# Optimization experiments

Hardware: AMD Instinct MI355X
Metric: run time of the kernel (lower is better)

The kernel has to match this reference:

```python
import jax, jax.numpy as jnp
import numpy as np

B, NCAP, LEN, CDF = 8, 4, 1024, 768
NUM, IDF = 1024, 512


def setup_inputs() -> dict:
    key = jax.random.key(0)
    k1, k2, k3 = jax.random.split(key, 3)
    obj = jax.random.normal(k1, (B, NUM, IDF), dtype=jnp.float32)
    text = jax.random.normal(k2, (B, NCAP, LEN, CDF), dtype=jnp.float32)
    # Linear(cdf=768 -> idf=512); kaiming-uniform-ish scale
    W = jax.random.normal(k3, (CDF, IDF), dtype=jnp.float32) / np.sqrt(CDF)
    b = jnp.zeros((IDF,), dtype=jnp.float32)
    return {"obj": obj, "text": text, "W": W, "b": b}


def reference(obj, text, W, b):
    # obj: [B, num, idf]; text: [B, 4, len, cdf]
    batch = text.shape[0]
    idf = obj.shape[2]
    # conv_context: Linear(cdf -> idf), then flatten captions: [B, L=4*len, idf]
    t = (jnp.einsum('bcle,ed->bcld', text, W) + b).reshape(batch, -1, idf)
    # unscaled, unmasked cross-attention scores: [B, num, L]
    attn = jnp.einsum('bnd,bld->bnl', obj, t)
    # softmax over the flattened text dim (nn.Softmax on 2D applies to last dim)
    attn = jax.nn.softmax(attn, axis=-1)
    # dropout(p=0.5) is identity in eval mode (deterministic reference)
    # weightedText = bmm(t^T, attn^T) then transpose -> [B, num, idf]
    out = jnp.einsum('bnl,bld->bnd', attn, t)
    return out
```

## Files before the change

kernel.cpp:

```cpp
#include <hip/hip_runtime.h>
#include <math.h>


typedef unsigned short u16;
typedef u16   u16x4  __attribute__((ext_vector_type(4)));
typedef u16   u16x8  __attribute__((ext_vector_type(8)));
typedef __bf16 bf16x8 __attribute__((ext_vector_type(8)));
typedef float f32x4  __attribute__((ext_vector_type(4)));

__device__ inline void split4(const float4 v, u16x4* h4, u16x4* l4) {
  const float xs[4] = {v.x, v.y, v.z, v.w};
  #pragma unroll
  for (int c = 0; c < 4; c++) {
    __bf16 hb = (__bf16)xs[c];
    __bf16 lb = (__bf16)(xs[c] - (float)hb);
    (*h4)[c] = __builtin_bit_cast(u16, hb);
    (*l4)[c] = __builtin_bit_cast(u16, lb);
  }
}

template<bool ADD_BIAS>
__global__ __launch_bounds__(256, 2) void gemm_nt_bf16x3(
    const float* __restrict__ A, const float* __restrict__ B,
    float* __restrict__ C, const float* __restrict__ bias,
    int M, int N, int K, long sA, long sB, long sC)
{
  __shared__ __align__(16) u16 Ah[2][128][40];
  __shared__ __align__(16) u16 Al[2][128][40];
  __shared__ __align__(16) u16 Bh[2][128][40];
  __shared__ __align__(16) u16 Bl[2][128][40];

  const float* Ab = A + (long)blockIdx.z * sA;
  const float* Bb = B + (long)blockIdx.z * sB;
  float*       Cb = C + (long)blockIdx.z * sC;

  const int m0 = blockIdx.y * 128;
  const int n0 = blockIdx.x * 128;
  const int t    = threadIdx.x;
  const int lane = t & 63;
  const int w    = t >> 6;
  const int wm   = w >> 1;
  const int wn   = w & 1;
  const int lr   = lane & 15;
  const int lg   = lane >> 4;

  f32x4 acc[4][4];
  #pragma unroll
  for (int i = 0; i < 4; i++)
    #pragma unroll
    for (int j = 0; j < 4; j++) acc[i][j] = (f32x4){0.f, 0.f, 0.f, 0.f};

  float4 av[4], bv[4];

  #define LOADK(K0)                                                                 \
    _Pragma("unroll")                                                               \
    for (int i = 0; i < 4; i++) {                                                   \
      const int f   = t + 256 * i;                                                  \
      const int row = f >> 3;                                                       \
      const int kq  = (f & 7) * 4;                                                  \
      av[i] = *reinterpret_cast<const float4*>(Ab + (long)(m0 + row) * K + (K0) + kq); \
      bv[i] = *reinterpret_cast<const float4*>(Bb + (long)(n0 + row) * K + (K0) + kq); \
    }

  #define CONVWRITE(BUF)                                                            \
    _Pragma("unroll")                                                               \
    for (int i = 0; i < 4; i++) {                                                   \
      const int f   = t + 256 * i;                                                  \
      const int row = f >> 3;                                                       \
      const int kq  = (f & 7) * 4;                                                  \
      u16x4 h4, l4;                                                                 \
      split4(av[i], &h4, &l4);                                                      \
      *reinterpret_cast<u16x4*>(&Ah[BUF][row][kq]) = h4;                            \
      *reinterpret_cast<u16x4*>(&Al[BUF][row][kq]) = l4;                            \
      split4(bv[i], &h4, &l4);                                                      \
      *reinterpret_cast<u16x4*>(&Bh[BUF][row][kq]) = h4;                            \
      *reinterpret_cast<u16x4*>(&Bl[BUF][row][kq]) = l4;                            \
    }

  LOADK(0)
  CONVWRITE(0)
  __syncthreads();

  const int nk = K >> 5;
  for (int kt = 0; kt < nk; ++kt) {
    const int cur = kt & 1;
    if (kt + 1 < nk) { LOADK((kt + 1) << 5) }

    bf16x8 afh[4], afl[4];
    #pragma unroll
    for (int i = 0; i < 4; i++) {
      const int ar = wm * 64 + i * 16 + lr;
      afh[i] = __builtin_bit_cast(bf16x8, *reinterpret_cast<const u16x8*>(&Ah[cur][ar][lg * 8]));
      afl[i] = __builtin_bit_cast(bf16x8, *reinterpret_cast<const u16x8*>(&Al[cur][ar][lg * 8]));
    }
    #pragma unroll
    for (int j = 0; j < 4; j++) {
      const int br = wn * 64 + j * 16 + lr;
      bf16x8 bh = __builtin_bit_cast(bf16x8, *reinterpret_cast<const u16x8*>(&Bh[cur][br][lg * 8]));
      bf16x8 bl = __builtin_bit_cast(bf16x8, *reinterpret_cast<const u16x8*>(&Bl[cur][br][lg * 8]));
      #pragma unroll
      for (int i = 0; i < 4; i++) {
        acc[i][j] = __builtin_amdgcn_mfma_f32_16x16x32_bf16(afl[i], bh, acc[i][j], 0, 0, 0);
        acc[i][j] = __builtin_amdgcn_mfma_f32_16x16x32_bf16(afh[i], bl, acc[i][j], 0, 0, 0);
        acc[i][j] = __builtin_amdgcn_mfma_f32_16x16x32_bf16(afh[i], bh, acc[i][j], 0, 0, 0);
      }
    }

    if (kt + 1 < nk) { CONVWRITE(cur ^ 1) }
    __syncthreads();
  }
  #undef LOADK
  #undef CONVWRITE

  #pragma unroll
  for (int j = 0; j < 4; j++) {
    const int col = n0 + wn * 64 + j * 16 + lr;
    const float bj = ADD_BIAS ? bias[col] : 0.f;
    #pragma unroll
    for (int i = 0; i < 4; i++) {
      const int row = m0 + wm * 64 + i * 16 + lg * 4;
      #pragma unroll
      for (int r = 0; r < 4; r++)
        Cb[(long)(row + r) * N + col] = acc[i][j][r] + bj;
    }
  }
}

__global__ __launch_bounds__(256) void transpose_f32(
    const float* __restrict__ in, float* __restrict__ out,
    int R, int C, long sIn, long sOut)
{
  __shared__ float tile[32][33];
  in  += (long)blockIdx.z * sIn;
  out += (long)blockIdx.z * sOut;
  const int c  = blockIdx.x * 32 + threadIdx.x;
  const int r0 = blockIdx.y * 32 + threadIdx.y;
  #pragma unroll
  for (int j = 0; j < 32; j += 8)
    tile[threadIdx.y + j][threadIdx.x] = in[(long)(r0 + j) * C + c];
  __syncthreads();
  const int c2 = blockIdx.y * 32 + threadIdx.x;
  const int r2 = blockIdx.x * 32 + threadIdx.y;
  #pragma unroll
  for (int j = 0; j < 32; j += 8)
    out[(long)(r2 + j) * R + c2] = tile[threadIdx.x][threadIdx.y + j];
}

__device__ inline float wave_max(float x) {
  #pragma unroll
  for (int o = 1; o < 64; o <<= 1) x = fmaxf(x, __shfl_xor(x, o, 64));
  return x;
}
__device__ inline float wave_sum(float x) {
  #pragma unroll
  for (int o = 1; o < 64; o <<= 1) x += __shfl_xor(x, o, 64);
  return x;
}

__global__ __launch_bounds__(256) void softmax4096_kernel(float* __restrict__ attn)
{
  __shared__ float red[4];
  float* p = attn + (long)blockIdx.x * 4096;
  const int t = threadIdx.x;

  float4 v[4];
  float mx = -3.4e38f;
  #pragma unroll
  for (int i = 0; i < 4; i++) {
    v[i] = *reinterpret_cast<const float4*>(p + i * 1024 + t * 4);
    mx = fmaxf(mx, fmaxf(fmaxf(v[i].x, v[i].y), fmaxf(v[i].z, v[i].w)));
  }
  mx = wave_max(mx);
  if ((t & 63) == 0) red[t >> 6] = mx;
  __syncthreads();
  mx = fmaxf(fmaxf(red[0], red[1]), fmaxf(red[2], red[3]));
  __syncthreads();

  float s = 0.f;
  #pragma unroll
  for (int i = 0; i < 4; i++) {
    v[i].x = __expf(v[i].x - mx); s += v[i].x;
    v[i].y = __expf(v[i].y - mx); s += v[i].y;
    v[i].z = __expf(v[i].z - mx); s += v[i].z;
    v[i].w = __expf(v[i].w - mx); s += v[i].w;
  }
  s = wave_sum(s);
  if ((t & 63) == 0) red[t >> 6] = s;
  __syncthreads();
  const float r = 1.f / (red[0] + red[1] + red[2] + red[3]);

  #pragma unroll
  for (int i = 0; i < 4; i++) {
    v[i].x *= r; v[i].y *= r; v[i].z *= r; v[i].w *= r;
    *reinterpret_cast<float4*>(p + i * 1024 + t * 4) = v[i];
  }
}

extern "C" void kernel_launch(void* const* d_in, const int* in_sizes, int n_in,
                              void* d_out, int out_size, void* d_ws, size_t ws_size,
                              hipStream_t stream)
{
  const float* obj  = (const float*)d_in[0];
  const float* text = (const float*)d_in[1];
  const float* W    = (const float*)d_in[2];
  const float* bias = (const float*)d_in[3];
  float*       out  = (float*)d_out;

  float* t    = (float*)d_ws;
  float* attn = t    + 32768L * 512;
  float* tT   = attn + 8L * 1024 * 4096;
  float* WT   = tT   + 8L * 512 * 4096;

  transpose_f32<<<dim3(512 / 32, 768 / 32, 1), dim3(32, 8), 0, stream>>>(
      W, WT, 768, 512, 0L, 0L);
  gemm_nt_bf16x3<true><<<dim3(512 / 128, 32768 / 128, 1), 256, 0, stream>>>(
      text, WT, t, bias, 32768, 512, 768, 0L, 0L, 0L);
  transpose_f32<<<dim3(512 / 32, 4096 / 32, 8), dim3(32, 8), 0, stream>>>(
      t, tT, 4096, 512, 4096L * 512, 512L * 4096);
  gemm_nt_bf16x3<false><<<dim3(4096 / 128, 1024 / 128, 8), 256, 0, stream>>>(
      obj, t, attn, nullptr, 1024, 4096, 512,
      1024L * 512, 4096L * 512, 1024L * 4096);
  softmax4096_kernel<<<8192, 256, 0, stream>>>(attn);
  gemm_nt_bf16x3<false><<<dim3(512 / 128, 1024 / 128, 8), 256, 0, stream>>>(
      attn, tT, out, nullptr, 1024, 512, 4096,
      1024L * 4096, 512L * 4096, 1024L * 512);
}
```

Measured before the change: 557.8 us.

## Pre-split operands to bf16 hi/lo in global memory and stage via direct-to-LDS loads

Operands are now converted once into separate bf16 high and low arrays in global memory by standalone split kernels, by the softmax, and by the first GEMM's epilogue. The GEMM then streams these arrays straight into swizzled LDS with global_load_lds, with each wave staging one of the four planes. This removes the per-tile float-to-bf16 split work and the register round-trip from the GEMM main loop, and the standalone transpose of t is dropped because the projection epilogue also writes the transposed t. The cost is extra kernel launches, extra global traffic to write and re-read the split copies, and a single workspace buffer reused for several tensors.

```diff
diff --git a/kernel.cpp b/kernel.cpp
--- a/kernel.cpp
+++ b/kernel.cpp
@@ -3,14 +3,14 @@
 
 
 typedef unsigned short u16;
-typedef u16   u16x4  __attribute__((ext_vector_type(4)));
-typedef u16   u16x8  __attribute__((ext_vector_type(8)));
+typedef u16 u16x4 __attribute__((ext_vector_type(4)));
+typedef u16 u16x8 __attribute__((ext_vector_type(8)));
 typedef __bf16 bf16x8 __attribute__((ext_vector_type(8)));
-typedef float f32x4  __attribute__((ext_vector_type(4)));
+typedef float f32x4 __attribute__((ext_vector_type(4)));
 
 __device__ inline void split4(const float4 v, u16x4* h4, u16x4* l4) {
   const float xs[4] = {v.x, v.y, v.z, v.w};
-  #pragma unroll
+#pragma unroll
   for (int c = 0; c < 4; c++) {
     __bf16 hb = (__bf16)xs[c];
     __bf16 lb = (__bf16)(xs[c] - (float)hb);
@@ -19,20 +19,22 @@
   }
 }
 
-template<bool ADD_BIAS>
-__global__ __launch_bounds__(256, 2) void gemm_nt_bf16x3(
-    const float* __restrict__ A, const float* __restrict__ B,
+__device__ inline void gload_lds16(const u16* g, u16* l) {
+  __builtin_amdgcn_global_load_lds(
+      (const __attribute__((address_space(1))) unsigned int*)g,
+      (__attribute__((address_space(3))) unsigned int*)l, 16, 0, 0);
+}
+
+template<int MODE>
+__global__ __launch_bounds__(256, 2) void gemm_x3(
+    const u16* __restrict__ Ah, const u16* __restrict__ Al,
+    const u16* __restrict__ Bh, const u16* __restrict__ Bl,
     float* __restrict__ C, const float* __restrict__ bias,
+    u16* __restrict__ th, u16* __restrict__ tl,
+    u16* __restrict__ tTh, u16* __restrict__ tTl,
     int M, int N, int K, long sA, long sB, long sC)
 {
-  __shared__ __align__(16) u16 Ah[2][128][40];
-  __shared__ __align__(16) u16 Al[2][128][40];
-  __shared__ __align__(16) u16 Bh[2][128][40];
-  __shared__ __align__(16) u16 Bl[2][128][40];
-
-  const float* Ab = A + (long)blockIdx.z * sA;
-  const float* Bb = B + (long)blockIdx.z * sB;
-  float*       Cb = C + (long)blockIdx.z * sC;
+  __shared__ __align__(16) u16 sh[4][2][4096];
 
   const int m0 = blockIdx.y * 128;
   const int n0 = blockIdx.x * 128;
@@ -44,128 +46,182 @@
   const int lr   = lane & 15;
   const int lg   = lane >> 4;
 
+  const u16* Abh = Ah + (long)blockIdx.z * sA;
+  const u16* Abl = Al + (long)blockIdx.z * sA;
+  const u16* Bbh = Bh + (long)blockIdx.z * sB;
+  const u16* Bbl = Bl + (long)blockIdx.z * sB;
+  float*     Cb  = C  + (long)blockIdx.z * sC;
+
+  const u16* wsrc; long wrow;
+  if      (w == 0) { wsrc = Abh; wrow = (long)m0 * K; }
+  else if (w == 1) { wsrc = Abl; wrow = (long)m0 * K; }
+  else if (w == 2) { wsrc = Bbh; wrow = (long)n0 * K; }
+  else             { wsrc = Bbl; wrow = (long)n0 * K; }
+
+  int offA[4], offB[4];
+#pragma unroll
+  for (int i = 0; i < 4; i++) {
+    const int ar = wm * 64 + i * 16 + lr;
+    offA[i] = ar * 32 + (((lg + (ar >> 1)) & 3) << 3);
+    const int br = wn * 64 + i * 16 + lr;
+    offB[i] = br * 32 + (((lg + (br >> 1)) & 3) << 3);
+  }
+
   f32x4 acc[4][4];
-  #pragma unroll
+#pragma unroll
   for (int i = 0; i < 4; i++)
-    #pragma unroll
+#pragma unroll
     for (int j = 0; j < 4; j++) acc[i][j] = (f32x4){0.f, 0.f, 0.f, 0.f};
 
-  float4 av[4], bv[4];
-
-  #define LOADK(K0)                                                                 \
-    _Pragma("unroll")                                                               \
-    for (int i = 0; i < 4; i++) {                                                   \
-      const int f   = t + 256 * i;                                                  \
-      const int row = f >> 3;                                                       \
-      const int kq  = (f & 7) * 4;                                                  \
-      av[i] = *reinterpret_cast<const float4*>(Ab + (long)(m0 + row) * K + (K0) + kq); \
-      bv[i] = *reinterpret_cast<const float4*>(Bb + (long)(n0 + row) * K + (K0) + kq); \
-    }
-
-  #define CONVWRITE(BUF)                                                            \
-    _Pragma("unroll")                                                               \
-    for (int i = 0; i < 4; i++) {                                                   \
-      const int f   = t + 256 * i;                                                  \
-      const int row = f >> 3;                                                       \
-      const int kq  = (f & 7) * 4;                                                  \
-      u16x4 h4, l4;                                                                 \
-      split4(av[i], &h4, &l4);                                                      \
-      *reinterpret_cast<u16x4*>(&Ah[BUF][row][kq]) = h4;                            \
-      *reinterpret_cast<u16x4*>(&Al[BUF][row][kq]) = l4;                            \
-      split4(bv[i], &h4, &l4);                                                      \
-      *reinterpret_cast<u16x4*>(&Bh[BUF][row][kq]) = h4;                            \
-      *reinterpret_cast<u16x4*>(&Bl[BUF][row][kq]) = l4;                            \
-    }
-
-  LOADK(0)
-  CONVWRITE(0)
+  #define STAGE(NB, K0)                                                        \
+    {                                                                          \
+      u16* lb = &sh[w][NB][0];                                                 \
+      _Pragma("unroll")                                                        \
+      for (int ii = 0; ii < 8; ii++) {                                         \
+        const int G  = ii * 64 + lane;                                         \
+        const int rr = G >> 2, qq = G & 3;                                     \
+        const int kq = (qq - (rr >> 1)) & 3;                                   \
+        gload_lds16(wsrc + wrow + (long)rr * K + (K0) + kq * 8, lb + ii * 512);\
+      }                                                                        \
+    }
+
+  STAGE(0, 0)
   __syncthreads();
 
   const int nk = K >> 5;
+  int cur = 0;
   for (int kt = 0; kt < nk; ++kt) {
-    const int cur = kt & 1;
-    if (kt + 1 < nk) { LOADK((kt + 1) << 5) }
-
-    bf16x8 afh[4], afl[4];
-    #pragma unroll
+    if (kt + 1 < nk) STAGE(cur ^ 1, (kt + 1) << 5)
+
+    const u16* P0 = &sh[0][cur][0];
+    const u16* P1 = &sh[1][cur][0];
+    const u16* P2 = &sh[2][cur][0];
+    const u16* P3 = &sh[3][cur][0];
+    bf16x8 ah[4], al[4], bh[4], bl[4];
+#pragma unroll
     for (int i = 0; i < 4; i++) {
-      const int ar = wm * 64 + i * 16 + lr;
-      afh[i] = __builtin_bit_cast(bf16x8, *reinterpret_cast<const u16x8*>(&Ah[cur][ar][lg * 8]));
-      afl[i] = __builtin_bit_cast(bf16x8, *reinterpret_cast<const u16x8*>(&Al[cur][ar][lg * 8]));
-    }
-    #pragma unroll
+      ah[i] = __builtin_bit_cast(bf16x8, *(const u16x8*)(P0 + offA[i]));
+      al[i] = __builtin_bit_cast(bf16x8, *(const u16x8*)(P1 + offA[i]));
+      bh[i] = __builtin_bit_cast(bf16x8, *(const u16x8*)(P2 + offB[i]));
+      bl[i] = __builtin_bit_cast(bf16x8, *(const u16x8*)(P3 + offB[i]));
+    }
+#pragma unroll
+    for (int i = 0; i < 4; i++)
+#pragma unroll
+      for (int j = 0; j < 4; j++)
+        acc[i][j] = __builtin_amdgcn_mfma_f32_16x16x32_bf16(al[i], bh[j], acc[i][j], 0, 0, 0);
+#pragma unroll
+    for (int i = 0; i < 4; i++)
+#pragma unroll
+      for (int j = 0; j < 4; j++)
+        acc[i][j] = __builtin_amdgcn_mfma_f32_16x16x32_bf16(ah[i], bl[j], acc[i][j], 0, 0, 0);
+#pragma unroll
+    for (int i = 0; i < 4; i++)
+#pragma unroll
+      for (int j = 0; j < 4; j++)
+        acc[i][j] = __builtin_amdgcn_mfma_f32_16x16x32_bf16(ah[i], bh[j], acc[i][j], 0, 0, 0);
+
+    __syncthreads();
+    cur ^= 1;
+  }
+  #undef STAGE
+
+  if (MODE == 0) {
+#pragma unroll
     for (int j = 0; j < 4; j++) {
-      const int br = wn * 64 + j * 16 + lr;
-      bf16x8 bh = __builtin_bit_cast(bf16x8, *reinterpret_cast<const u16x8*>(&Bh[cur][br][lg * 8]));
-      bf16x8 bl = __builtin_bit_cast(bf16x8, *reinterpret_cast<const u16x8*>(&Bl[cur][br][lg * 8]));
-      #pragma unroll
+      const int col = n0 + wn * 64 + j * 16 + lr;
+#pragma unroll
       for (int i = 0; i < 4; i++) {
-        acc[i][j] = __builtin_amdgcn_mfma_f32_16x16x32_bf16(afl[i], bh, acc[i][j], 0, 0, 0);
-        acc[i][j] = __builtin_amdgcn_mfma_f32_16x16x32_bf16(afh[i], bl, acc[i][j], 0, 0, 0);
-        acc[i][j] = __builtin_amdgcn_mfma_f32_16x16x32_bf16(afh[i], bh, acc[i][j], 0, 0, 0);
+        const int row = m0 + wm * 64 + i * 16 + lg * 4;
+#pragma unroll
+        for (int r = 0; r < 4; r++)
+          Cb[(long)(row + r) * N + col] = acc[i][j][r];
       }
     }
-
-    if (kt + 1 < nk) { CONVWRITE(cur ^ 1) }
-    __syncthreads();
-  }
-  #undef LOADK
-  #undef CONVWRITE
-
-  #pragma unroll
-  for (int j = 0; j < 4; j++) {
-    const int col = n0 + wn * 64 + j * 16 + lr;
-    const float bj = ADD_BIAS ? bias[col] : 0.f;
-    #pragma unroll
-    for (int i = 0; i < 4; i++) {
-      const int row = m0 + wm * 64 + i * 16 + lg * 4;
-      #pragma unroll
-      for (int r = 0; r < 4; r++)
-        Cb[(long)(row + r) * N + col] = acc[i][j][r] + bj;
-    }
-  }
-}
-
-__global__ __launch_bounds__(256) void transpose_f32(
-    const float* __restrict__ in, float* __restrict__ out,
-    int R, int C, long sIn, long sOut)
+  } else {
+#pragma unroll
+    for (int j = 0; j < 4; j++) {
+      const int col = n0 + wn * 64 + j * 16 + lr;
+      const float bj = bias[col];
+#pragma unroll
+      for (int i = 0; i < 4; i++) {
+        const int row = m0 + wm * 64 + i * 16 + lg * 4;
+        float4 vv;
+        vv.x = acc[i][j][0] + bj; vv.y = acc[i][j][1] + bj;
+        vv.z = acc[i][j][2] + bj; vv.w = acc[i][j][3] + bj;
+        u16x4 h4, l4;
+        split4(vv, &h4, &l4);
+#pragma unroll
+        for (int r = 0; r < 4; r++) {
+          th[(long)(row + r) * 512 + col] = h4[r];
+          tl[(long)(row + r) * 512 + col] = l4[r];
+        }
+        const int b = row >> 12, rl = row & 4095;
+        const long ti = (long)b * (512L * 4096) + (long)col * 4096 + rl;
+        *(u16x4*)(tTh + ti) = h4;
+        *(u16x4*)(tTl + ti) = l4;
+      }
+    }
+  }
+}
+
+__global__ __launch_bounds__(256) void split_pair(
+    const float* __restrict__ in, u16* __restrict__ h, u16* __restrict__ l, long n4)
+{
+  for (long i = blockIdx.x * 256 + threadIdx.x; i < n4; i += (long)gridDim.x * 256) {
+    float4 v = ((const float4*)in)[i];
+    u16x4 h4, l4;
+    split4(v, &h4, &l4);
+    ((u16x4*)h)[i] = h4;
+    ((u16x4*)l)[i] = l4;
+  }
+}
+
+__global__ __launch_bounds__(256) void prep_W(
+    const float* __restrict__ W, u16* __restrict__ WTh, u16* __restrict__ WTl)
 {
   __shared__ float tile[32][33];
-  in  += (long)blockIdx.z * sIn;
-  out += (long)blockIdx.z * sOut;
   const int c  = blockIdx.x * 32 + threadIdx.x;
   const int r0 = blockIdx.y * 32 + threadIdx.y;
-  #pragma unroll
+#pragma unroll
   for (int j = 0; j < 32; j += 8)
-    tile[threadIdx.y + j][threadIdx.x] = in[(long)(r0 + j) * C + c];
+    tile[threadIdx.y + j][threadIdx.x] = W[(r0 + j) * 512 + c];
   __syncthreads();
   const int c2 = blockIdx.y * 32 + threadIdx.x;
   const int r2 = blockIdx.x * 32 + threadIdx.y;
-  #pragma unroll
-  for (int j = 0; j < 32; j += 8)
-    out[(long)(r2 + j) * R + c2] = tile[threadIdx.x][threadIdx.y + j];
+#pragma unroll
+  for (int j = 0; j < 32; j += 8) {
+    const float v = tile[threadIdx.x][threadIdx.y + j];
+    const __bf16 hb = (__bf16)v;
+    const __bf16 lb = (__bf16)(v - (float)hb);
+    WTh[(r2 + j) * 768 + c2] = __builtin_bit_cast(u16, hb);
+    WTl[(r2 + j) * 768 + c2] = __builtin_bit_cast(u16, lb);
+  }
 }
 
 __device__ inline float wave_max(float x) {
-  #pragma unroll
+#pragma unroll
   for (int o = 1; o < 64; o <<= 1) x = fmaxf(x, __shfl_xor(x, o, 64));
   return x;
 }
 __device__ inline float wave_sum(float x) {
-  #pragma unroll
+#pragma unroll
   for (int o = 1; o < 64; o <<= 1) x += __shfl_xor(x, o, 64);
   return x;
 }
 
-__global__ __launch_bounds__(256) void softmax4096_kernel(float* __restrict__ attn)
+__global__ __launch_bounds__(256) void softmax4096_hl(
+    const float* __restrict__ attn, u16* __restrict__ ah, u16* __restrict__ al)
 {
   __shared__ float red[4];
-  float* p = attn + (long)blockIdx.x * 4096;
+  const float* p = attn + (long)blockIdx.x * 4096;
+  u16* ph = ah + (long)blockIdx.x * 4096;
+  u16* pl = al + (long)blockIdx.x * 4096;
   const int t = threadIdx.x;
 
   float4 v[4];
   float mx = -3.4e38f;
-  #pragma unroll
+#pragma unroll
   for (int i = 0; i < 4; i++) {
     v[i] = *reinterpret_cast<const float4*>(p + i * 1024 + t * 4);
     mx = fmaxf(mx, fmaxf(fmaxf(v[i].x, v[i].y), fmaxf(v[i].z, v[i].w)));
@@ -177,7 +233,7 @@
   __syncthreads();
 
   float s = 0.f;
-  #pragma unroll
+#pragma unroll
   for (int i = 0; i < 4; i++) {
     v[i].x = __expf(v[i].x - mx); s += v[i].x;
     v[i].y = __expf(v[i].y - mx); s += v[i].y;
@@ -189,10 +245,13 @@
   __syncthreads();
   const float r = 1.f / (red[0] + red[1] + red[2] + red[3]);
 
-  #pragma unroll
+#pragma unroll
   for (int i = 0; i < 4; i++) {
     v[i].x *= r; v[i].y *= r; v[i].z *= r; v[i].w *= r;
-    *reinterpret_cast<float4*>(p + i * 1024 + t * 4) = v[i];
+    u16x4 h4, l4;
+    split4(v[i], &h4, &l4);
+    *(u16x4*)(ph + i * 1024 + t * 4) = h4;
+    *(u16x4*)(pl + i * 1024 + t * 4) = l4;
   }
 }
 
@@ -206,22 +265,33 @@
   const float* bias = (const float*)d_in[3];
   float*       out  = (float*)d_out;
 
-  float* t    = (float*)d_ws;
-  float* attn = t    + 32768L * 512;
-  float* tT   = attn + 8L * 1024 * 4096;
-  float* WT   = tT   + 8L * 512 * 4096;
-
-  transpose_f32<<<dim3(512 / 32, 768 / 32, 1), dim3(32, 8), 0, stream>>>(
-      W, WT, 768, 512, 0L, 0L);
-  gemm_nt_bf16x3<true><<<dim3(512 / 128, 32768 / 128, 1), 256, 0, stream>>>(
-      text, WT, t, bias, 32768, 512, 768, 0L, 0L, 0L);
-  transpose_f32<<<dim3(512 / 32, 4096 / 32, 8), dim3(32, 8), 0, stream>>>(
-      t, tT, 4096, 512, 4096L * 512, 512L * 4096);
-  gemm_nt_bf16x3<false><<<dim3(4096 / 128, 1024 / 128, 8), 256, 0, stream>>>(
-      obj, t, attn, nullptr, 1024, 4096, 512,
-      1024L * 512, 4096L * 512, 1024L * 4096);
-  softmax4096_kernel<<<8192, 256, 0, stream>>>(attn);
-  gemm_nt_bf16x3<false><<<dim3(512 / 128, 1024 / 128, 8), 256, 0, stream>>>(
-      attn, tT, out, nullptr, 1024, 512, 4096,
-      1024L * 4096, 512L * 4096, 1024L * 512);
-}
+  char* base = (char*)d_ws;
+  const long MB = 1024L * 1024;
+  u16* text_h = (u16*)(base + 0 * MB);
+  u16* text_l = (u16*)(base + 48 * MB);
+  u16* obj_h  = (u16*)(base + 96 * MB);
+  u16* obj_l  = (u16*)(base + 104 * MB);
+  u16* t_h    = (u16*)(base + 112 * MB);
+  u16* t_l    = (u16*)(base + 144 * MB);
+  u16* tT_h   = (u16*)(base + 176 * MB);
+  u16* tT_l   = (u16*)(base + 208 * MB);
+  u16* WT_h   = (u16*)(base + 240 * MB);
+  u16* WT_l   = (u16*)(base + 241 * MB);
+  float* attn_f32 = (float*)(base + 242 * MB);
+  u16* attn_h = (u16*)(base + 0 * MB);
+  u16* attn_l = (u16*)(base + 64 * MB);
+
+  prep_W<<<dim3(16, 24), dim3(32, 8), 0, stream>>>(W, WT_h, WT_l);
+  split_pair<<<2048, 256, 0, stream>>>(text, text_h, text_l, 32768L * 768 / 4);
+  split_pair<<<2048, 256, 0, stream>>>(obj, obj_h, obj_l, 8192L * 512 / 4);
+  gemm_x3<1><<<dim3(4, 256, 1), 256, 0, stream>>>(
+      text_h, text_l, WT_h, WT_l, nullptr, bias, t_h, t_l, tT_h, tT_l,
+      32768, 512, 768, 0L, 0L, 0L);
+  gemm_x3<0><<<dim3(32, 8, 8), 256, 0, stream>>>(
+      obj_h, obj_l, t_h, t_l, attn_f32, nullptr, nullptr, nullptr, nullptr, nullptr,
+      1024, 4096, 512, 1024L * 512, 4096L * 512, 1024L * 4096);
+  softmax4096_hl<<<8192, 256, 0, stream>>>(attn_f32, attn_h, attn_l);
+  gemm_x3<0><<<dim3(4, 8, 8), 256, 0, stream>>>(
+      attn_h, attn_l, tT_h, tT_l, out, nullptr, nullptr, nullptr, nullptr, nullptr,
+      1024, 512, 4096, 1024L * 4096, 512L * 4096, 1024L * 512);
+}
```

After: 755.3 us. +35.4%, slower.
